# Kernel optimization log

Measured on AMD Instinct MI355X. Metric: run time of the kernel, lower is better.

## Reference

```python
import jax, jax.numpy as jnp
import numpy as np
from jax import lax

B, T, IN, H = 4096, 512, 11, 16


def lstm(x, Wih, Whh, bih, bhh):
    # x: [B, T, in]; PyTorch gate order i, f, g, o packed along 4H.
    xg = jnp.einsum('bti,gi->btg', x, Wih) + bih + bhh  # [B, T, 4H]
    h0 = jnp.zeros((x.shape[0], Whh.shape[1]), x.dtype)
    c0 = jnp.zeros_like(h0)

    def step(carry, xg_t):
        h, c = carry
        g = xg_t + h @ Whh.T                      # [B, 4H]
        i, f, gg, o = jnp.split(g, 4, axis=-1)
        i = jax.nn.sigmoid(i)
        f = jax.nn.sigmoid(f)
        gg = jnp.tanh(gg)
        o = jax.nn.sigmoid(o)
        c = f * c + i * gg
        h = o * jnp.tanh(c)
        return (h, c), h

    _, hs = lax.scan(step, (h0, c0), jnp.swapaxes(xg, 0, 1))  # hs: [T, B, H]
    return jnp.swapaxes(hs, 0, 1)  # [B, T, H]


def setup_inputs() -> dict:
    key = jax.random.key(0)
    ks = jax.random.split(key, 16)
    s = 1.0 / np.sqrt(H)
    u = lambda k, shape: jax.random.uniform(k, shape, jnp.float32, -s, s)
    return {
        'x': jax.random.normal(ks[0], (B, T, IN), jnp.float32),
        'Wih1': u(ks[1], (4 * H, IN)), 'Whh1': u(ks[2], (4 * H, H)),
        'bih1': u(ks[3], (4 * H,)), 'bhh1': u(ks[4], (4 * H,)),
        'Wih2': u(ks[5], (4 * H, H)), 'Whh2': u(ks[6], (4 * H, H)),
        'bih2': u(ks[7], (4 * H,)), 'bhh2': u(ks[8], (4 * H,)),
        'Wd1': u(ks[9], (8, H)), 'bd1': u(ks[10], (8,)),
        'Wd2': u(ks[11], (8, 8)), 'bd2': u(ks[12], (8,)),
        'Wd3': u(ks[13], (3, 8)), 'bd3': u(ks[14], (3,)),
    }


def reference(x, Wih1, Whh1, bih1, bhh1, Wih2, Whh2, bih2, bhh2,
              Wd1, bd1, Wd2, bd2, Wd3, bd3):
    h1 = lstm(x, Wih1, Whh1, bih1, bhh1)          # [B, T, H]
    # Dropout2d treated as identity (eval mode).
    h2 = lstm(h1, Wih2, Whh2, bih2, bhh2)          # [B, T, H]
    s = jax.nn.softmax(h2, axis=1)[:, -1, :]       # softmax over TIME, take last step -> [B, H]
    d = (s @ Wd1.T + bd1) @ Wd2.T + bd2
    d = d @ Wd3.T + bd3                            # [B, 3]
    return jax.nn.softmax(d, axis=1)
```

## Files before the change

kernel.cpp:

```cpp
#include <hip/hip_runtime.h>

#define T_STEPS 512
#define IN_DIM 11
#define ROW_PAD 12
#define H_DIM 16
#define ROW_F (T_STEPS * IN_DIM)
#define CHUNK_T 16
#define CHUNK_F (CHUNK_T * IN_DIM)
#define N_CHUNK (T_STEPS / CHUNK_T)
#define LOG2E 1.44269504088896340736f

typedef _Float16 v2h __attribute__((ext_vector_type(2)));
typedef _Float16 v4h __attribute__((ext_vector_type(4)));

__device__ __forceinline__ float fdot2(v2h a, v2h b, float c) {
    return __builtin_amdgcn_fdot2(a, b, c, false);
}
__device__ __forceinline__ v2h as_v2h(int v) { return __builtin_bit_cast(v2h, v); }

template<int CTRL>
__device__ __forceinline__ float qperm(float v) {
    return __builtin_bit_cast(float,
        __builtin_amdgcn_update_dpp(0, __builtin_bit_cast(int, v),
                                    CTRL, 0xf, 0xf, true));
}

__device__ __forceinline__ float bcast_lane(float v, int l) {
    return __builtin_bit_cast(float,
        __builtin_amdgcn_readlane(__builtin_bit_cast(int, v), l));
}

__global__ __launch_bounds__(256)
__attribute__((amdgpu_waves_per_eu(4, 4)))
void lstm2_head(
    const float* __restrict__ x,
    const float* __restrict__ Wih1, const float* __restrict__ Whh1,
    const float* __restrict__ bih1, const float* __restrict__ bhh1,
    const float* __restrict__ Wih2, const float* __restrict__ Whh2,
    const float* __restrict__ bih2, const float* __restrict__ bhh2,
    const float* __restrict__ Wd1, const float* __restrict__ bd1,
    const float* __restrict__ Wd2, const float* __restrict__ bd2,
    const float* __restrict__ Wd3, const float* __restrict__ bd3,
    float* __restrict__ out)
{
    __shared__ __align__(16) _Float16 xlds[4][2][216];

    const int lane = threadIdx.x & 63;
    const int wid = __builtin_amdgcn_readfirstlane((int)(threadIdx.x >> 6));
    const int b = blockIdx.x * 4 + wid;

    const int r   = lane >> 2;
    const int gt  = lane & 3;
    const int row = gt * H_DIM + r;

    const bool is_t = (gt == 2);
    const float M   = is_t ? (-2.0f * LOG2E) : (-LOG2E);
    const float vAa = is_t ? 2.0f : 1.0f;
    const float vBc = is_t ? -1.0f : 0.0f;

    v2h wi1h[6], wh1h[8], wi2h[8], wh2h[8];
    #pragma unroll
    for (int j = 0; j < 5; ++j)
        wi1h[j] = (v2h){(_Float16)(M * Wih1[row * IN_DIM + 2 * j]),
                        (_Float16)(M * Wih1[row * IN_DIM + 2 * j + 1])};
    wi1h[5] = (v2h){(_Float16)(M * Wih1[row * IN_DIM + 10]), (_Float16)0.0f};
    #pragma unroll
    for (int j = 0; j < 8; ++j) {
        wh1h[j] = (v2h){(_Float16)(M * Whh1[row * H_DIM + 2 * j]),
                        (_Float16)(M * Whh1[row * H_DIM + 2 * j + 1])};
        wi2h[j] = (v2h){(_Float16)(M * Wih2[row * H_DIM + 2 * j]),
                        (_Float16)(M * Wih2[row * H_DIM + 2 * j + 1])};
        wh2h[j] = (v2h){(_Float16)(M * Whh2[row * H_DIM + 2 * j]),
                        (_Float16)(M * Whh2[row * H_DIM + 2 * j + 1])};
    }
    const float bb1 = M * (bih1[row] + bhh1[row]);
    const float bb2 = M * (bih2[row] + bhh2[row]);
    #pragma unroll
    for (int j = 0; j < 6; ++j) asm volatile("" : "+v"(wi1h[j]));
    #pragma unroll
    for (int j = 0; j < 8; ++j) {
        asm volatile("" : "+v"(wh1h[j]));
        asm volatile("" : "+v"(wi2h[j]));
        asm volatile("" : "+v"(wh2h[j]));
    }

    const float* __restrict__ xb = x + (size_t)b * ROW_F;
    _Float16* const xl0 = &xlds[wid][0][0];
    _Float16* const xl1 = &xlds[wid][1][0];

    if (lane < 32) {
        const int buf = lane >> 4, rr = lane & 15;
        xlds[wid][buf][rr * ROW_PAD + IN_DIM] = (_Float16)0.0f;
    }

    const int f1i = lane, f2i = lane + 64, f3i = lane + 128;
    const int p1 = (f1i / IN_DIM) * ROW_PAD + (f1i % IN_DIM);
    const int p2 = (f2i / IN_DIM) * ROW_PAD + (f2i % IN_DIM);
    const int p3 = (f3i / IN_DIM) * ROW_PAD + (f3i % IN_DIM);

    float gl0 = xb[f1i];
    float gl1 = xb[f2i];
    float gl2 = xb[min(f3i, ROW_F - 1)];

    float c1 = 0.f, c2 = 0.f, h2v = 0.f, ssum = 0.f;
    int h1p[8], h2p[8];
    #pragma unroll
    for (int j = 0; j < 8; ++j) { h1p[j] = 0; h2p[j] = 0; }

    #define HPACK(HV, DST)                                                      \
        {                                                                       \
            const int lo_ = __builtin_bit_cast(int,                             \
                __builtin_amdgcn_cvt_pkrtz(HV, HV));                            \
            const int hi_ = __builtin_amdgcn_update_dpp(0, lo_, 0x104,          \
                                                        0xf, 0xf, true);        \
            const int pk_ = (lo_ & 0xFFFF) | (hi_ & (int)0xFFFF0000u);          \
            _Pragma("unroll")                                                   \
            for (int j = 0; j < 8; ++j)                                         \
                DST[j] = __builtin_amdgcn_readlane(pk_, 8 * j);                 \
        }

    for (int ck = 0; ck < N_CHUNK; ++ck) {
        _Float16* const xbuf = (ck & 1) ? xl1 : xl0;
        xbuf[p1] = (_Float16)gl0;
        xbuf[p2] = (_Float16)gl1;
        xbuf[p3] = (_Float16)gl2;
        if (ck + 1 < N_CHUNK) {
            const int base = (ck + 1) * CHUNK_F;
            gl0 = xb[base + f1i];
            gl1 = xb[base + f2i];
            gl2 = xb[min(base + f3i, ROW_F - 1)];
        }

        #pragma unroll
        for (int t2 = 0; t2 < CHUNK_T; ++t2) {
            const v4h* const xr4 = (const v4h*)(xbuf + t2 * ROW_PAD);

            float a2 = bb2, b2 = 0.f;
            #pragma unroll
            for (int j = 0; j < 4; ++j) {
                a2 = fdot2(wh2h[j],     as_v2h(h2p[j]),     a2);
                b2 = fdot2(wh2h[j + 4], as_v2h(h2p[j + 4]), b2);
            }

            const v4h x0 = xr4[0], x1 = xr4[1], x2 = xr4[2];
            float a1 = bb1, b1 = 0.f;
            a1 = fdot2(wi1h[0], __builtin_shufflevector(x0, x0, 0, 1), a1);
            b1 = fdot2(wi1h[1], __builtin_shufflevector(x0, x0, 2, 3), b1);
            a1 = fdot2(wi1h[2], __builtin_shufflevector(x1, x1, 0, 1), a1);
            b1 = fdot2(wi1h[3], __builtin_shufflevector(x1, x1, 2, 3), b1);
            a1 = fdot2(wi1h[4], __builtin_shufflevector(x2, x2, 0, 1), a1);
            b1 = fdot2(wi1h[5], __builtin_shufflevector(x2, x2, 2, 3), b1);
            #pragma unroll
            for (int j = 0; j < 4; ++j) {
                a1 = fdot2(wh1h[j],     as_v2h(h1p[j]),     a1);
                b1 = fdot2(wh1h[j + 4], as_v2h(h1p[j + 4]), b1);
            }

            const float g1 = a1 + b1;
            const float act1 = __builtin_fmaf(vAa,
                __builtin_amdgcn_rcpf(1.0f + __builtin_amdgcn_exp2f(g1)), vBc);
            float h1v;
            {
                const float gi = qperm<0x00>(act1);
                const float gf = qperm<0x55>(act1);
                const float gg = qperm<0xAA>(act1);
                const float go = qperm<0xFF>(act1);
                c1 = __builtin_fmaf(gf, c1, gi * gg);
                const float tc = __builtin_fmaf(2.0f,
                    __builtin_amdgcn_rcpf(1.0f +
                        __builtin_amdgcn_exp2f(-2.0f * LOG2E * c1)), -1.0f);
                h1v = go * tc;
            }
            HPACK(h1v, h1p)

            #pragma unroll
            for (int j = 0; j < 4; ++j) {
                a2 = fdot2(wi2h[j],     as_v2h(h1p[j]),     a2);
                b2 = fdot2(wi2h[j + 4], as_v2h(h1p[j + 4]), b2);
            }

            const float g2 = a2 + b2;
            const float act2 = __builtin_fmaf(vAa,
                __builtin_amdgcn_rcpf(1.0f + __builtin_amdgcn_exp2f(g2)), vBc);
            {
                const float gi = qperm<0x00>(act2);
                const float gf = qperm<0x55>(act2);
                const float gg = qperm<0xAA>(act2);
                const float go = qperm<0xFF>(act2);
                c2 = __builtin_fmaf(gf, c2, gi * gg);
                const float tc = __builtin_fmaf(2.0f,
                    __builtin_amdgcn_rcpf(1.0f +
                        __builtin_amdgcn_exp2f(-2.0f * LOG2E * c2)), -1.0f);
                h2v = go * tc;
            }
            HPACK(h2v, h2p)

            ssum += __builtin_amdgcn_exp2f(LOG2E * h2v);
        }
    }
    #undef HPACK

    const float sv = __builtin_amdgcn_exp2f(LOG2E * h2v) / ssum;

    float ssb[H_DIM];
    #pragma unroll
    for (int k = 0; k < H_DIM; ++k) ssb[k] = bcast_lane(sv, 4 * k);

    const int r8 = lane & 7;
    float acc1 = bd1[r8];
    #pragma unroll
    for (int k = 0; k < H_DIM; ++k)
        acc1 = __builtin_fmaf(Wd1[r8 * H_DIM + k], ssb[k], acc1);

    float d1s[8];
    #pragma unroll
    for (int j = 0; j < 8; ++j) d1s[j] = bcast_lane(acc1, j);

    float acc2 = bd2[r8];
    #pragma unroll
    for (int k = 0; k < 8; ++k)
        acc2 = __builtin_fmaf(Wd2[r8 * 8 + k], d1s[k], acc2);

    float d2s[8];
    #pragma unroll
    for (int j = 0; j < 8; ++j) d2s[j] = bcast_lane(acc2, j);

    float lg = 0.f;
    if (lane < 3) {
        lg = bd3[lane];
        #pragma unroll
        for (int k = 0; k < 8; ++k)
            lg = __builtin_fmaf(Wd3[lane * 8 + k], d2s[k], lg);
    }
    const float l0 = bcast_lane(lg, 0);
    const float l1 = bcast_lane(lg, 1);
    const float l2 = bcast_lane(lg, 2);
    const float mx = fmaxf(l0, fmaxf(l1, l2));
    const float e0 = __builtin_amdgcn_exp2f(LOG2E * (l0 - mx));
    const float e1 = __builtin_amdgcn_exp2f(LOG2E * (l1 - mx));
    const float e2 = __builtin_amdgcn_exp2f(LOG2E * (l2 - mx));
    const float inv = 1.0f / (e0 + e1 + e2);
    if (lane < 3) {
        const float ev = (lane == 0) ? e0 : ((lane == 1) ? e1 : e2);
        out[b * 3 + lane] = ev * inv;
    }
}

extern "C" void kernel_launch(void* const* d_in, const int* in_sizes, int n_in,
                              void* d_out, int out_size, void* d_ws, size_t ws_size,
                              hipStream_t stream) {
    (void)in_sizes; (void)n_in; (void)out_size; (void)d_ws; (void)ws_size;
    const float* x    = (const float*)d_in[0];
    const float* Wih1 = (const float*)d_in[1];
    const float* Whh1 = (const float*)d_in[2];
    const float* bih1 = (const float*)d_in[3];
    const float* bhh1 = (const float*)d_in[4];
    const float* Wih2 = (const float*)d_in[5];
    const float* Whh2 = (const float*)d_in[6];
    const float* bih2 = (const float*)d_in[7];
    const float* bhh2 = (const float*)d_in[8];
    const float* Wd1  = (const float*)d_in[9];
    const float* bd1  = (const float*)d_in[10];
    const float* Wd2  = (const float*)d_in[11];
    const float* bd2  = (const float*)d_in[12];
    const float* Wd3  = (const float*)d_in[13];
    const float* bd3  = (const float*)d_in[14];

    lstm2_head<<<dim3(4096 / 4), dim3(256), 0, stream>>>(
        x, Wih1, Whh1, bih1, bhh1, Wih2, Whh2, bih2, bhh2,
        Wd1, bd1, Wd2, bd2, Wd3, bd3, (float*)d_out);
}
```

Before: 497.4 us.

## Broadcast LSTM hidden state through LDS and use packed fp16 FMA accumulation

Each step now writes its hidden-state value to a small per-wave LDS buffer and reads it back as two 8-wide fp16 vectors. This replaces the cvt/DPP pack plus eight readlane broadcasts per layer. The recurrent matrix-vector products switch from fp32-accumulating fdot2 chains to packed fp16 FMA chains, reduced at the end with a single fdot2 against ones. The tanh-gate activation constants are rescaled so the cell state is kept pre-multiplied by -2*log2(e), which removes one multiply before each exp2. This trades readlane latency for an LDS round trip and adds fp16 accumulation error in the recurrence.

```diff
diff --git a/kernel.cpp b/kernel.cpp
--- a/kernel.cpp
+++ b/kernel.cpp
@@ -12,11 +12,21 @@
 
 typedef _Float16 v2h __attribute__((ext_vector_type(2)));
 typedef _Float16 v4h __attribute__((ext_vector_type(4)));
+typedef _Float16 v8h __attribute__((ext_vector_type(8)));
 
 __device__ __forceinline__ float fdot2(v2h a, v2h b, float c) {
     return __builtin_amdgcn_fdot2(a, b, c, false);
 }
-__device__ __forceinline__ v2h as_v2h(int v) { return __builtin_bit_cast(v2h, v); }
+__device__ __forceinline__ v2h pk_fma_h(v2h a, v2h b, v2h c) {
+    v2h d;
+    asm("v_pk_fma_f16 %0, %1, %2, %3" : "=v"(d) : "v"(a), "v"(b), "v"(c));
+    return d;
+}
+__device__ __forceinline__ v2h pk_add_h(v2h a, v2h b) {
+    v2h d;
+    asm("v_pk_add_f16 %0, %1, %2" : "=v"(d) : "v"(a), "v"(b));
+    return d;
+}
 
 template<int CTRL>
 __device__ __forceinline__ float qperm(float v) {
@@ -29,6 +39,8 @@
     return __builtin_bit_cast(float,
         __builtin_amdgcn_readlane(__builtin_bit_cast(int, v), l));
 }
+
+#define HS(V, J) ((v2h){(V)[2 * (J)], (V)[2 * (J) + 1]})
 
 __global__ __launch_bounds__(256)
 __attribute__((amdgpu_waves_per_eu(4, 4)))
@@ -44,6 +56,7 @@
     float* __restrict__ out)
 {
     __shared__ __align__(16) _Float16 xlds[4][2][216];
+    __shared__ __align__(16) _Float16 hsl[4][2][16];
 
     const int lane = threadIdx.x & 63;
     const int wid = __builtin_amdgcn_readfirstlane((int)(threadIdx.x >> 6));
@@ -55,8 +68,8 @@
 
     const bool is_t = (gt == 2);
     const float M   = is_t ? (-2.0f * LOG2E) : (-LOG2E);
-    const float vAa = is_t ? 2.0f : 1.0f;
-    const float vBc = is_t ? -1.0f : 0.0f;
+    const float vAa = is_t ? (-4.0f * LOG2E) : 1.0f;
+    const float vBc = is_t ? (2.0f * LOG2E) : 0.0f;
 
     v2h wi1h[6], wh1h[8], wi2h[8], wh2h[8];
     #pragma unroll
@@ -87,7 +100,10 @@
     const float* __restrict__ xb = x + (size_t)b * ROW_F;
     _Float16* const xl0 = &xlds[wid][0][0];
     _Float16* const xl1 = &xlds[wid][1][0];
-
+    _Float16* const h1w = &hsl[wid][0][0];
+    _Float16* const h2w = &hsl[wid][1][0];
+
+    if (lane < 32) hsl[wid][lane >> 4][lane & 15] = (_Float16)0.0f;
     if (lane < 32) {
         const int buf = lane >> 4, rr = lane & 15;
         xlds[wid][buf][rr * ROW_PAD + IN_DIM] = (_Float16)0.0f;
@@ -103,21 +119,9 @@
     float gl2 = xb[min(f3i, ROW_F - 1)];
 
     float c1 = 0.f, c2 = 0.f, h2v = 0.f, ssum = 0.f;
-    int h1p[8], h2p[8];
-    #pragma unroll
-    for (int j = 0; j < 8; ++j) { h1p[j] = 0; h2p[j] = 0; }
-
-    #define HPACK(HV, DST)                                                      \
-        {                                                                       \
-            const int lo_ = __builtin_bit_cast(int,                             \
-                __builtin_amdgcn_cvt_pkrtz(HV, HV));                            \
-            const int hi_ = __builtin_amdgcn_update_dpp(0, lo_, 0x104,          \
-                                                        0xf, 0xf, true);        \
-            const int pk_ = (lo_ & 0xFFFF) | (hi_ & (int)0xFFFF0000u);          \
-            _Pragma("unroll")                                                   \
-            for (int j = 0; j < 8; ++j)                                         \
-                DST[j] = __builtin_amdgcn_readlane(pk_, 8 * j);                 \
-        }
+    v8h h1a = {}, h1b = {}, h2a = {}, h2b = {};
+    const v2h ones = (v2h){(_Float16)1.0f, (_Float16)1.0f};
+    const v2h z2   = (v2h){(_Float16)0.0f, (_Float16)0.0f};
 
     for (int ck = 0; ck < N_CHUNK; ++ck) {
         _Float16* const xbuf = (ck & 1) ? xl1 : xl0;
@@ -133,33 +137,38 @@
 
         #pragma unroll
         for (int t2 = 0; t2 < CHUNK_T; ++t2) {
-            const v4h* const xr4 = (const v4h*)(xbuf + t2 * ROW_PAD);
-
-            float a2 = bb2, b2 = 0.f;
-            #pragma unroll
-            for (int j = 0; j < 4; ++j) {
-                a2 = fdot2(wh2h[j],     as_v2h(h2p[j]),     a2);
-                b2 = fdot2(wh2h[j + 4], as_v2h(h2p[j + 4]), b2);
-            }
-
+            v2h p0 = pk_fma_h(wh2h[0], HS(h2a, 0), z2);
+            v2h q0 = pk_fma_h(wh2h[4], HS(h2b, 0), z2);
+            p0 = pk_fma_h(wh2h[1], HS(h2a, 1), p0);
+            q0 = pk_fma_h(wh2h[5], HS(h2b, 1), q0);
+            p0 = pk_fma_h(wh2h[2], HS(h2a, 2), p0);
+            q0 = pk_fma_h(wh2h[6], HS(h2b, 2), q0);
+            p0 = pk_fma_h(wh2h[3], HS(h2a, 3), p0);
+            q0 = pk_fma_h(wh2h[7], HS(h2b, 3), q0);
+            const v2h hc2 = pk_add_h(p0, q0);
+
+            const v4h* xr4 = (const v4h*)(xbuf + t2 * ROW_PAD);
             const v4h x0 = xr4[0], x1 = xr4[1], x2 = xr4[2];
             float a1 = bb1, b1 = 0.f;
-            a1 = fdot2(wi1h[0], __builtin_shufflevector(x0, x0, 0, 1), a1);
-            b1 = fdot2(wi1h[1], __builtin_shufflevector(x0, x0, 2, 3), b1);
-            a1 = fdot2(wi1h[2], __builtin_shufflevector(x1, x1, 0, 1), a1);
-            b1 = fdot2(wi1h[3], __builtin_shufflevector(x1, x1, 2, 3), b1);
-            a1 = fdot2(wi1h[4], __builtin_shufflevector(x2, x2, 0, 1), a1);
-            b1 = fdot2(wi1h[5], __builtin_shufflevector(x2, x2, 2, 3), b1);
-            #pragma unroll
-            for (int j = 0; j < 4; ++j) {
-                a1 = fdot2(wh1h[j],     as_v2h(h1p[j]),     a1);
-                b1 = fdot2(wh1h[j + 4], as_v2h(h1p[j + 4]), b1);
-            }
-
-            const float g1 = a1 + b1;
+            a1 = fdot2(wi1h[0], (v2h){x0[0], x0[1]}, a1);
+            b1 = fdot2(wi1h[1], (v2h){x0[2], x0[3]}, b1);
+            a1 = fdot2(wi1h[2], (v2h){x1[0], x1[1]}, a1);
+            b1 = fdot2(wi1h[3], (v2h){x1[2], x1[3]}, b1);
+            a1 = fdot2(wi1h[4], (v2h){x2[0], x2[1]}, a1);
+            b1 = fdot2(wi1h[5], (v2h){x2[2], x2[3]}, b1);
+
+            v2h u0 = pk_fma_h(wh1h[0], HS(h1a, 0), z2);
+            v2h u1 = pk_fma_h(wh1h[4], HS(h1b, 0), z2);
+            u0 = pk_fma_h(wh1h[1], HS(h1a, 1), u0);
+            u1 = pk_fma_h(wh1h[5], HS(h1b, 1), u1);
+            u0 = pk_fma_h(wh1h[2], HS(h1a, 2), u0);
+            u1 = pk_fma_h(wh1h[6], HS(h1b, 2), u1);
+            u0 = pk_fma_h(wh1h[3], HS(h1a, 3), u0);
+            u1 = pk_fma_h(wh1h[7], HS(h1b, 3), u1);
+            const float g1 = fdot2(ones, pk_add_h(u0, u1), a1 + b1);
+
             const float act1 = __builtin_fmaf(vAa,
                 __builtin_amdgcn_rcpf(1.0f + __builtin_amdgcn_exp2f(g1)), vBc);
-            float h1v;
             {
                 const float gi = qperm<0x00>(act1);
                 const float gf = qperm<0x55>(act1);
@@ -167,19 +176,24 @@
                 const float go = qperm<0xFF>(act1);
                 c1 = __builtin_fmaf(gf, c1, gi * gg);
                 const float tc = __builtin_fmaf(2.0f,
-                    __builtin_amdgcn_rcpf(1.0f +
-                        __builtin_amdgcn_exp2f(-2.0f * LOG2E * c1)), -1.0f);
-                h1v = go * tc;
+                    __builtin_amdgcn_rcpf(1.0f + __builtin_amdgcn_exp2f(c1)),
+                    -1.0f);
+                h1w[r] = (_Float16)(go * tc);
             }
-            HPACK(h1v, h1p)
-
-            #pragma unroll
-            for (int j = 0; j < 4; ++j) {
-                a2 = fdot2(wi2h[j],     as_v2h(h1p[j]),     a2);
-                b2 = fdot2(wi2h[j + 4], as_v2h(h1p[j + 4]), b2);
-            }
-
-            const float g2 = a2 + b2;
+            h1a = ((const v8h*)h1w)[0];
+            h1b = ((const v8h*)h1w)[1];
+
+            v2h v0 = pk_fma_h(wi2h[0], HS(h1a, 0), z2);
+            v2h v1 = pk_fma_h(wi2h[4], HS(h1b, 0), z2);
+            v0 = pk_fma_h(wi2h[1], HS(h1a, 1), v0);
+            v1 = pk_fma_h(wi2h[5], HS(h1b, 1), v1);
+            v0 = pk_fma_h(wi2h[2], HS(h1a, 2), v0);
+            v1 = pk_fma_h(wi2h[6], HS(h1b, 2), v1);
+            v0 = pk_fma_h(wi2h[3], HS(h1a, 3), v0);
+            v1 = pk_fma_h(wi2h[7], HS(h1b, 3), v1);
+            const float g2 = fdot2(ones,
+                pk_add_h(hc2, pk_add_h(v0, v1)), bb2);
+
             const float act2 = __builtin_fmaf(vAa,
                 __builtin_amdgcn_rcpf(1.0f + __builtin_amdgcn_exp2f(g2)), vBc);
             {
@@ -189,16 +203,17 @@
                 const float go = qperm<0xFF>(act2);
                 c2 = __builtin_fmaf(gf, c2, gi * gg);
                 const float tc = __builtin_fmaf(2.0f,
-                    __builtin_amdgcn_rcpf(1.0f +
-                        __builtin_amdgcn_exp2f(-2.0f * LOG2E * c2)), -1.0f);
+                    __builtin_amdgcn_rcpf(1.0f + __builtin_amdgcn_exp2f(c2)),
+                    -1.0f);
                 h2v = go * tc;
+                h2w[r] = (_Float16)h2v;
             }
-            HPACK(h2v, h2p)
+            h2a = ((const v8h*)h2w)[0];
+            h2b = ((const v8h*)h2w)[1];
 
             ssum += __builtin_amdgcn_exp2f(LOG2E * h2v);
         }
     }
-    #undef HPACK
 
     const float sv = __builtin_amdgcn_exp2f(LOG2E * h2v) / ssum;
 
```

Result: faster. 468.5 us (-5.8%).
